# Kernel optimization log

Measured on AMD Instinct MI355X. Metric: run time of the kernel, lower is better.

The kernel has to match this reference:

```python
import jax, jax.numpy as jnp
import numpy as np

B, S, H = 2, 2048, 2048
FFN = 1024
E = 8
TOP_K = 2


def setup_inputs() -> dict:
    key = jax.random.key(0)
    ks = jax.random.split(key, 5)
    scale = 0.02
    hidden_states = jax.random.normal(ks[0], (B, S, H), dtype=jnp.float32)
    Wg = jax.random.normal(ks[1], (E, H), dtype=jnp.float32) * scale   # gate: Linear(H, E) weight
    W1 = jax.random.normal(ks[2], (E, FFN, H), dtype=jnp.float32) * scale  # stacked w1 per expert
    W3 = jax.random.normal(ks[3], (E, FFN, H), dtype=jnp.float32) * scale  # stacked w3 per expert
    W2 = jax.random.normal(ks[4], (E, H, FFN), dtype=jnp.float32) * scale  # stacked w2 per expert
    bias = jnp.zeros((E,), dtype=jnp.float32)  # e_score_correction_bias buffer
    return {"hidden_states": hidden_states, "Wg": Wg, "W1": W1, "W2": W2, "W3": W3, "bias": bias}


def reference(hidden_states, Wg, W1, W2, W3, bias):
    bsz, seq_len, hidden_dim = hidden_states.shape
    x = hidden_states.reshape(-1, hidden_dim)                 # [T, H]
    router_logits = x @ Wg.T                                  # [T, E]
    routing_weights = jax.nn.sigmoid(router_logits.astype(jnp.float32))
    scores = routing_weights + bias                           # bias only affects selection
    _, top_k_index = jax.lax.top_k(scores, TOP_K)             # [T, K]
    top_k_weights = jnp.take_along_axis(routing_weights, top_k_index, axis=1)
    top_k_weights = top_k_weights / top_k_weights.sum(axis=-1, keepdims=True)
    top_k_weights = top_k_weights.astype(x.dtype)
    # per-token per-expert combine weight (0 for non-selected experts)
    one_hot = jax.nn.one_hot(top_k_index, Wg.shape[0], dtype=x.dtype)  # [T, K, E]
    expert_w = jnp.einsum('tk,tke->te', top_k_weights, one_hot)        # [T, E]
    # SwiGLU expert MLPs applied via stacked (grouped) GEMMs
    h1 = jnp.einsum('th,efh->tef', x, W1)                     # [T, E, FFN]
    h3 = jnp.einsum('th,efh->tef', x, W3)
    g = jax.nn.silu(h1) * h3 * expert_w[:, :, None]           # scale before down-proj
    out = jnp.einsum('tef,ehf->th', g, W2)                    # weighted combine
    return out.reshape(bsz, seq_len, hidden_dim)
```

## Files before the change

kernel.cpp:

```cpp
#include <hip/hip_runtime.h>
#include <hip/hip_bf16.h>


#define T_TOK 4096
#define H_DIM 2048
#define FFN_D 1024
#define NE    8

typedef __attribute__((ext_vector_type(8))) short          bf16x8;
typedef __attribute__((ext_vector_type(4))) float          f32x4;
typedef __attribute__((ext_vector_type(4))) unsigned short us4;

__device__ __forceinline__ unsigned short f2bf(float f) {
  unsigned u = __builtin_bit_cast(unsigned, f);
  u += 0x7fffu + ((u >> 16) & 1u);
  return (unsigned short)(u >> 16);
}
__device__ __forceinline__ float bf2f(unsigned short u) {
  return __builtin_bit_cast(float, ((unsigned)u) << 16);
}
__device__ __forceinline__ void async16(const void* g, void* l) {
  __builtin_amdgcn_global_load_lds((const __attribute__((address_space(1))) void*)g,
                                   (__attribute__((address_space(3))) void*)l, 16, 0, 0);
}

__global__ void router2_kernel(const float* __restrict__ x,
                               const float* __restrict__ Wg,
                               const float* __restrict__ bias,
                               unsigned* __restrict__ epair,
                               float* __restrict__ wpair,
                               unsigned short* __restrict__ Xb) {
  const int wv   = threadIdx.x >> 6;
  const int lane = threadIdx.x & 63;
  const int t    = blockIdx.x * 4 + wv;

  const float4* xr = (const float4*)(x + (size_t)t * H_DIM);
  us4*          xb = (us4*)(Xb + (size_t)t * H_DIM);

  float acc[NE];
#pragma unroll
  for (int e = 0; e < NE; e++) acc[e] = 0.f;

#pragma unroll
  for (int j = 0; j < 8; j++) {
    int i4 = j * 64 + lane;
    float4 v = xr[i4];
    us4 d; d.x = f2bf(v.x); d.y = f2bf(v.y); d.z = f2bf(v.z); d.w = f2bf(v.w);
    xb[i4] = d;
#pragma unroll
    for (int e = 0; e < NE; e++) {
      float4 w = ((const float4*)(Wg + e * H_DIM))[i4];
      acc[e] += v.x * w.x + v.y * w.y + v.z * w.z + v.w * w.w;
    }
  }
#pragma unroll
  for (int e = 0; e < NE; e++) {
#pragma unroll
    for (int m = 32; m >= 1; m >>= 1) acc[e] += __shfl_xor(acc[e], m, 64);
  }

  if (lane == 0) {
    float sig[NE], sc[NE];
#pragma unroll
    for (int e = 0; e < NE; e++) {
      sig[e] = 1.f / (1.f + expf(-acc[e]));
      sc[e]  = sig[e] + bias[e];
    }
    int i1 = 0; float v1 = sc[0];
#pragma unroll
    for (int e = 1; e < NE; e++) if (sc[e] > v1) { v1 = sc[e]; i1 = e; }
    int i2 = -1; float v2 = -1e30f;
#pragma unroll
    for (int e = 0; e < NE; e++) if (e != i1 && sc[e] > v2) { v2 = sc[e]; i2 = e; }
    float w1 = sig[i1], w2 = sig[i2];
    float s = w1 + w2;
    epair[t] = (unsigned)i1 | ((unsigned)i2 << 8);
    wpair[2 * t]     = w1 / s;
    wpair[2 * t + 1] = w2 / s;
  }
}

#define N4_PER_W ((size_t)NE * FFN_D * H_DIM / 4)
#define NB_CONV  ((unsigned)(3 * N4_PER_W / 512))

__global__ void convert_all_kernel(const float* __restrict__ W1, unsigned short* __restrict__ W1b,
                                   const float* __restrict__ W3, unsigned short* __restrict__ W3b,
                                   const float* __restrict__ W2, unsigned short* __restrict__ W2b,
                                   const unsigned* __restrict__ epair,
                                   const float* __restrict__ wpair,
                                   int* __restrict__ cnt, int* __restrict__ base,
                                   int* __restrict__ rows, float* __restrict__ wts,
                                   int* __restrict__ t2s) {
  if (blockIdx.x < NB_CONV) {
    size_t i = (size_t)blockIdx.x * 512 + threadIdx.x;
    const float* s; unsigned short* d;
    if (i < N4_PER_W)            { s = W1; d = W1b; }
    else if (i < 2 * N4_PER_W)   { s = W3; d = W3b; i -= N4_PER_W; }
    else                         { s = W2; d = W2b; i -= 2 * N4_PER_W; }
    float4 v = ((const float4*)s)[i];
    us4 o; o.x = f2bf(v.x); o.y = f2bf(v.y); o.z = f2bf(v.z); o.w = f2bf(v.w);
    ((us4*)d)[i] = o;
    return;
  }
  const int e    = threadIdx.x >> 6;
  const int lane = threadIdx.x & 63;
  const unsigned long long ltmask = ((unsigned long long)1 << lane) - 1;
  __shared__ int cnts[NE];

  int count = 0;
  for (int c = 0; c < T_TOK; c += 64) {
    int t = c + lane;
    unsigned ep = epair[t];
    bool m1 = ((ep & 255u) == (unsigned)e);
    bool m2 = (((ep >> 8) & 255u) == (unsigned)e);
    unsigned long long b1 = __ballot(m1);
    if (m1) {
      int p = count + __popcll(b1 & ltmask);
      rows[e * T_TOK + p] = t;
      wts [e * T_TOK + p] = wpair[2 * t];
      t2s[2 * t] = (e << 12) | p;
    }
    count += __popcll(b1);
    unsigned long long b2 = __ballot(m2);
    if (m2) {
      int p = count + __popcll(b2 & ltmask);
      rows[e * T_TOK + p] = t;
      wts [e * T_TOK + p] = wpair[2 * t + 1];
      t2s[2 * t + 1] = (e << 12) | p;
    }
    count += __popcll(b2);
  }
  if (lane == 0) { cnts[e] = count; cnt[e] = count; }
  __syncthreads();
  if (threadIdx.x == 0) {
    int s = 0;
    for (int i = 0; i < NE; i++) { base[i] = s; s += cnts[i]; }
    base[NE] = s;
  }
}

__launch_bounds__(256)
__global__ void upproj_fast(const unsigned short* __restrict__ Xb,
                            const unsigned short* __restrict__ W1b,
                            const unsigned short* __restrict__ W3b,
                            const int* __restrict__ cnt,
                            const int* __restrict__ base,
                            const int* __restrict__ rows,
                            const float* __restrict__ wts,
                            unsigned short* __restrict__ G) {
  const int e  = blockIdx.z;
  const int m0 = blockIdx.y * 128;
  const int n0 = blockIdx.x * 64;
  const int ce = cnt[e];
  if (m0 >= ce) return;

  __shared__ __align__(16) unsigned short As [128 * 32];
  __shared__ __align__(16) unsigned short B1s[64 * 32];
  __shared__ __align__(16) unsigned short B3s[64 * 32];
  __shared__ int   t_ids[128];
  __shared__ float w_lds[128];

  const int tid = threadIdx.x;
  if (tid < 128) {
    int i = m0 + tid;
    if (i < ce) { t_ids[tid] = rows[e * T_TOK + i]; w_lds[tid] = wts[e * T_TOK + i]; }
    else        { t_ids[tid] = 0;                   w_lds[tid] = 0.f; }
  }
  __syncthreads();

  const int lane = tid & 63;
  const int wv   = tid >> 6;

  const unsigned short* gA[2];
#pragma unroll
  for (int c = 0; c < 2; c++) {
    int r = wv * 32 + c * 16 + (lane >> 2);
    gA[c] = Xb + (size_t)t_ids[r] * H_DIM + (lane & 3) * 8;
  }
  const size_t wrow = (size_t)(n0 + wv * 16 + (lane >> 2));
  const unsigned short* gB1 = W1b + (size_t)e * FFN_D * H_DIM + wrow * H_DIM + (lane & 3) * 8;
  const unsigned short* gB3 = W3b + (size_t)e * FFN_D * H_DIM + wrow * H_DIM + (lane & 3) * 8;
  unsigned short* lA0 = &As [(wv * 32 + 0)  * 32];
  unsigned short* lA1 = &As [(wv * 32 + 16) * 32];
  unsigned short* lB1 = &B1s[(wv * 16) * 32];
  unsigned short* lB3 = &B3s[(wv * 16) * 32];

  const int wm = (wv & 1) * 64;
  const int wn = (wv >> 1) * 32;
  const int qk = (lane >> 4) * 8;
  const int lr = lane & 15;

  f32x4 acc1[4][2], acc3[4][2];
#pragma unroll
  for (int mi = 0; mi < 4; mi++)
#pragma unroll
    for (int ni = 0; ni < 2; ni++) { acc1[mi][ni] = (f32x4)0.f; acc3[mi][ni] = (f32x4)0.f; }

  for (int kt = 0; kt < H_DIM; kt += 32) {
    async16(gA[0] + kt, lA0);
    async16(gA[1] + kt, lA1);
    async16(gB1 + kt,   lB1);
    async16(gB3 + kt,   lB3);
    __syncthreads();

    bf16x8 a[4], b1[2], b3[2];
#pragma unroll
    for (int mi = 0; mi < 4; mi++)
      a[mi] = *(const bf16x8*)&As[(wm + mi * 16 + lr) * 32 + qk];
#pragma unroll
    for (int ni = 0; ni < 2; ni++) {
      b1[ni] = *(const bf16x8*)&B1s[(wn + ni * 16 + lr) * 32 + qk];
      b3[ni] = *(const bf16x8*)&B3s[(wn + ni * 16 + lr) * 32 + qk];
    }
#pragma unroll
    for (int mi = 0; mi < 4; mi++)
#pragma unroll
      for (int ni = 0; ni < 2; ni++) {
        acc1[mi][ni] = __builtin_amdgcn_mfma_f32_16x16x32_bf16(a[mi], b1[ni], acc1[mi][ni], 0, 0, 0);
        acc3[mi][ni] = __builtin_amdgcn_mfma_f32_16x16x32_bf16(a[mi], b3[ni], acc3[mi][ni], 0, 0, 0);
      }
    __syncthreads();
  }

  const int be = base[e];
#pragma unroll
  for (int mi = 0; mi < 4; mi++)
#pragma unroll
    for (int ni = 0; ni < 2; ni++)
#pragma unroll
      for (int r = 0; r < 4; r++) {
        int row = wm + mi * 16 + (lane >> 4) * 4 + r;
        int col = wn + ni * 16 + lr;
        int i = m0 + row;
        if (i < ce) {
          float h1 = acc1[mi][ni][r];
          float h3 = acc3[mi][ni][r];
          float g  = h1 / (1.f + expf(-h1)) * h3 * w_lds[row];
          G[(size_t)(be + i) * FFN_D + n0 + col] = f2bf(g);
        }
      }
}

__launch_bounds__(256)
__global__ void downproj_fast(const unsigned short* __restrict__ G,
                              const unsigned short* __restrict__ W2b,
                              const int* __restrict__ cnt,
                              const int* __restrict__ base,
                              unsigned short* __restrict__ Gd) {
  const int e  = blockIdx.z;
  const int m0 = blockIdx.y * 128;
  const int n0 = blockIdx.x * 128;
  const int ce = cnt[e];
  if (m0 >= ce) return;
  const int be = base[e];

  __shared__ __align__(16) unsigned short As[128 * 32];
  __shared__ __align__(16) unsigned short Bs[128 * 32];

  const int tid  = threadIdx.x;
  const int lane = tid & 63;
  const int wv   = tid >> 6;

  const unsigned short* gA[2];
  const unsigned short* gB[2];
#pragma unroll
  for (int c = 0; c < 2; c++) {
    int r = m0 + wv * 32 + c * 16 + (lane >> 2);
    if (r >= ce) r = ce - 1;
    gA[c] = G + (size_t)(be + r) * FFN_D + (lane & 3) * 8;
    int rb = wv * 32 + c * 16 + (lane >> 2);
    gB[c] = W2b + (size_t)e * H_DIM * FFN_D + (size_t)(n0 + rb) * FFN_D + (lane & 3) * 8;
  }
  unsigned short* lA[2] = { &As[(wv * 32 + 0) * 32], &As[(wv * 32 + 16) * 32] };
  unsigned short* lB[2] = { &Bs[(wv * 32 + 0) * 32], &Bs[(wv * 32 + 16) * 32] };

  const int wm = (wv & 1) * 64;
  const int wn = (wv >> 1) * 64;
  const int qk = (lane >> 4) * 8;
  const int lr = lane & 15;

  f32x4 acc[4][4];
#pragma unroll
  for (int mi = 0; mi < 4; mi++)
#pragma unroll
    for (int ni = 0; ni < 4; ni++) acc[mi][ni] = (f32x4)0.f;

  for (int kt = 0; kt < FFN_D; kt += 32) {
    async16(gA[0] + kt, lA[0]);
    async16(gA[1] + kt, lA[1]);
    async16(gB[0] + kt, lB[0]);
    async16(gB[1] + kt, lB[1]);
    __syncthreads();

    bf16x8 a[4], b[4];
#pragma unroll
    for (int mi = 0; mi < 4; mi++)
      a[mi] = *(const bf16x8*)&As[(wm + mi * 16 + lr) * 32 + qk];
#pragma unroll
    for (int ni = 0; ni < 4; ni++)
      b[ni] = *(const bf16x8*)&Bs[(wn + ni * 16 + lr) * 32 + qk];
#pragma unroll
    for (int mi = 0; mi < 4; mi++)
#pragma unroll
      for (int ni = 0; ni < 4; ni++)
        acc[mi][ni] = __builtin_amdgcn_mfma_f32_16x16x32_bf16(a[mi], b[ni], acc[mi][ni], 0, 0, 0);
    __syncthreads();
  }

#pragma unroll
  for (int mi = 0; mi < 4; mi++)
#pragma unroll
    for (int ni = 0; ni < 4; ni++)
#pragma unroll
      for (int r = 0; r < 4; r++) {
        int row = wm + mi * 16 + (lane >> 4) * 4 + r;
        int col = wn + ni * 16 + lr;
        int i = m0 + row;
        if (i < ce)
          Gd[(size_t)(be + i) * H_DIM + n0 + col] = f2bf(acc[mi][ni][r]);
      }
}

__global__ void combine_kernel(const unsigned short* __restrict__ Gd,
                               const int* __restrict__ base,
                               const int* __restrict__ tok2slot,
                               float* __restrict__ out) {
  const int t = blockIdx.x;
  const int v1 = tok2slot[2 * t], v2 = tok2slot[2 * t + 1];
  const int s1 = base[v1 >> 12] + (v1 & 4095);
  const int s2 = base[v2 >> 12] + (v2 & 4095);
  const us4* r1 = (const us4*)(Gd + (size_t)s1 * H_DIM);
  const us4* r2 = (const us4*)(Gd + (size_t)s2 * H_DIM);
  float4* o = (float4*)(out + (size_t)t * H_DIM);
#pragma unroll
  for (int j = 0; j < 2; j++) {
    int i = j * 256 + threadIdx.x;
    us4 a = r1[i], b = r2[i];
    float4 r;
    r.x = bf2f(a.x) + bf2f(b.x);
    r.y = bf2f(a.y) + bf2f(b.y);
    r.z = bf2f(a.z) + bf2f(b.z);
    r.w = bf2f(a.w) + bf2f(b.w);
    o[i] = r;
  }
}

extern "C" void kernel_launch(void* const* d_in, const int* in_sizes, int n_in,
                              void* d_out, int out_size, void* d_ws, size_t ws_size,
                              hipStream_t stream) {
  (void)in_sizes; (void)n_in; (void)out_size; (void)ws_size;
  const float* x    = (const float*)d_in[0];
  const float* Wg   = (const float*)d_in[1];
  const float* W1   = (const float*)d_in[2];
  const float* W2   = (const float*)d_in[3];
  const float* W3   = (const float*)d_in[4];
  const float* bias = (const float*)d_in[5];
  float* out = (float*)d_out;

  char* ws = (char*)d_ws;
  const size_t OFF_CNT   = 0;
  const size_t OFF_BASE  = 64;
  const size_t OFF_T2S   = 1024;
  const size_t OFF_ROWS  = 65536;
  const size_t OFF_WTS   = OFF_ROWS + 131072;
  const size_t OFF_EPAIR = OFF_WTS + 131072;
  const size_t OFF_WPAIR = OFF_EPAIR + 16384;
  const size_t OFF_XB    = 1048576;
  const size_t OFF_W1B   = OFF_XB + 16777216;
  const size_t OFF_W3B   = OFF_W1B + 33554432;
  const size_t OFF_G     = OFF_W3B + 33554432;
  const size_t OFF_W2B   = OFF_G + 16777216;

  int*   cnt   = (int*)(ws + OFF_CNT);
  int*   base  = (int*)(ws + OFF_BASE);
  int*   t2s   = (int*)(ws + OFF_T2S);
  int*   rows  = (int*)(ws + OFF_ROWS);
  float* wts   = (float*)(ws + OFF_WTS);
  unsigned* epair = (unsigned*)(ws + OFF_EPAIR);
  float* wpair = (float*)(ws + OFF_WPAIR);
  unsigned short* Xb  = (unsigned short*)(ws + OFF_XB);
  unsigned short* W1b = (unsigned short*)(ws + OFF_W1B);
  unsigned short* W3b = (unsigned short*)(ws + OFF_W3B);
  unsigned short* W2b = (unsigned short*)(ws + OFF_W2B);
  unsigned short* Gd  = (unsigned short*)(ws + OFF_W1B);
  unsigned short* G   = (unsigned short*)(ws + OFF_G);

  router2_kernel<<<T_TOK / 4, 256, 0, stream>>>(x, Wg, bias, epair, wpair, Xb);

  convert_all_kernel<<<NB_CONV + 1, 512, 0, stream>>>(W1, W1b, W3, W3b, W2, W2b,
                                                      epair, wpair, cnt, base, rows, wts, t2s);

  dim3 g2(FFN_D / 64, T_TOK / 128, NE);
  upproj_fast<<<g2, 256, 0, stream>>>(Xb, W1b, W3b, cnt, base, rows, wts, G);

  dim3 g3(H_DIM / 128, T_TOK / 128, NE);
  downproj_fast<<<g3, 256, 0, stream>>>(G, W2b, cnt, base, Gd);

  combine_kernel<<<T_TOK, 256, 0, stream>>>(Gd, base, t2s, out);
}
```

Before: 461.5 us.

## Overlap weight conversion with router and up-projection kernels

Moves the W1/W3 fp32-to-bf16 conversion into the router kernel as extra blocks, and the W2 conversion into the up-projection launch as an extra z-slice, so conversion runs alongside routing and the GEMM. The compaction step becomes its own single-block kernel. This removes the serial dependency where all weight conversion had to finish before routing compaction and the up-projection could start. The trade-off is that the W2 conversion blocks now compete with GEMM blocks for CUs and memory bandwidth, and there is one extra small kernel launch.

```diff
diff --git a/kernel.cpp b/kernel.cpp
--- a/kernel.cpp
+++ b/kernel.cpp
@@ -11,6 +11,10 @@
 typedef __attribute__((ext_vector_type(4))) float          f32x4;
 typedef __attribute__((ext_vector_type(4))) unsigned short us4;
 
+#define N4_PER_W ((size_t)NE * FFN_D * H_DIM / 4)
+#define RB_ROUTER 1024u
+#define CB_CONV   8192u
+
 __device__ __forceinline__ unsigned short f2bf(float f) {
   unsigned u = __builtin_bit_cast(unsigned, f);
   u += 0x7fffu + ((u >> 16) & 1u);
@@ -24,12 +28,27 @@
                                    (__attribute__((address_space(3))) void*)l, 16, 0, 0);
 }
 
-__global__ void router2_kernel(const float* __restrict__ x,
-                               const float* __restrict__ Wg,
-                               const float* __restrict__ bias,
-                               unsigned* __restrict__ epair,
-                               float* __restrict__ wpair,
-                               unsigned short* __restrict__ Xb) {
+__global__ void router_conv_kernel(const float* __restrict__ x,
+                                   const float* __restrict__ Wg,
+                                   const float* __restrict__ bias,
+                                   unsigned* __restrict__ epair,
+                                   float* __restrict__ wpair,
+                                   unsigned short* __restrict__ Xb,
+                                   const float* __restrict__ W1, unsigned short* __restrict__ W1b,
+                                   const float* __restrict__ W3, unsigned short* __restrict__ W3b) {
+  if (blockIdx.x >= RB_ROUTER) {
+    size_t b0 = (size_t)(blockIdx.x - RB_ROUTER) * 1024;
+#pragma unroll
+    for (int k = 0; k < 4; k++) {
+      size_t i = b0 + k * 256 + threadIdx.x;
+      const float* s; unsigned short* d;
+      if (i < N4_PER_W) { s = W1; d = W1b; } else { s = W3; d = W3b; i -= N4_PER_W; }
+      float4 v = ((const float4*)s)[i];
+      us4 o; o.x = f2bf(v.x); o.y = f2bf(v.y); o.z = f2bf(v.z); o.w = f2bf(v.w);
+      ((us4*)d)[i] = o;
+    }
+    return;
+  }
   const int wv   = threadIdx.x >> 6;
   const int lane = threadIdx.x & 63;
   const int t    = blockIdx.x * 4 + wv;
@@ -80,28 +99,13 @@
   }
 }
 
-#define N4_PER_W ((size_t)NE * FFN_D * H_DIM / 4)
-#define NB_CONV  ((unsigned)(3 * N4_PER_W / 512))
-
-__global__ void convert_all_kernel(const float* __restrict__ W1, unsigned short* __restrict__ W1b,
-                                   const float* __restrict__ W3, unsigned short* __restrict__ W3b,
-                                   const float* __restrict__ W2, unsigned short* __restrict__ W2b,
-                                   const unsigned* __restrict__ epair,
-                                   const float* __restrict__ wpair,
-                                   int* __restrict__ cnt, int* __restrict__ base,
-                                   int* __restrict__ rows, float* __restrict__ wts,
-                                   int* __restrict__ t2s) {
-  if (blockIdx.x < NB_CONV) {
-    size_t i = (size_t)blockIdx.x * 512 + threadIdx.x;
-    const float* s; unsigned short* d;
-    if (i < N4_PER_W)            { s = W1; d = W1b; }
-    else if (i < 2 * N4_PER_W)   { s = W3; d = W3b; i -= N4_PER_W; }
-    else                         { s = W2; d = W2b; i -= 2 * N4_PER_W; }
-    float4 v = ((const float4*)s)[i];
-    us4 o; o.x = f2bf(v.x); o.y = f2bf(v.y); o.z = f2bf(v.z); o.w = f2bf(v.w);
-    ((us4*)d)[i] = o;
-    return;
-  }
+__global__ void compact_kernel(const unsigned* __restrict__ epair,
+                               const float* __restrict__ wpair,
+                               int* __restrict__ cnt,
+                               int* __restrict__ base,
+                               int* __restrict__ rows,
+                               float* __restrict__ wts,
+                               int* __restrict__ t2s) {
   const int e    = threadIdx.x >> 6;
   const int lane = threadIdx.x & 63;
   const unsigned long long ltmask = ((unsigned long long)1 << lane) - 1;
@@ -147,7 +151,20 @@
                             const int* __restrict__ base,
                             const int* __restrict__ rows,
                             const float* __restrict__ wts,
-                            unsigned short* __restrict__ G) {
+                            unsigned short* __restrict__ G,
+                            const float* __restrict__ W2, unsigned short* __restrict__ W2b) {
+  if (blockIdx.z == NE) {
+    size_t flat = (size_t)blockIdx.y * 16 + blockIdx.x;
+    size_t b0 = flat * 8192;
+#pragma unroll
+    for (int k = 0; k < 32; k++) {
+      size_t i = b0 + (size_t)k * 256 + threadIdx.x;
+      float4 v = ((const float4*)W2)[i];
+      us4 o; o.x = f2bf(v.x); o.y = f2bf(v.y); o.z = f2bf(v.z); o.w = f2bf(v.w);
+      ((us4*)W2b)[i] = o;
+    }
+    return;
+  }
   const int e  = blockIdx.z;
   const int m0 = blockIdx.y * 128;
   const int n0 = blockIdx.x * 64;
@@ -385,13 +402,13 @@
   unsigned short* Gd  = (unsigned short*)(ws + OFF_W1B);
   unsigned short* G   = (unsigned short*)(ws + OFF_G);
 
-  router2_kernel<<<T_TOK / 4, 256, 0, stream>>>(x, Wg, bias, epair, wpair, Xb);
-
-  convert_all_kernel<<<NB_CONV + 1, 512, 0, stream>>>(W1, W1b, W3, W3b, W2, W2b,
-                                                      epair, wpair, cnt, base, rows, wts, t2s);
-
-  dim3 g2(FFN_D / 64, T_TOK / 128, NE);
-  upproj_fast<<<g2, 256, 0, stream>>>(Xb, W1b, W3b, cnt, base, rows, wts, G);
+  router_conv_kernel<<<RB_ROUTER + CB_CONV, 256, 0, stream>>>(
+      x, Wg, bias, epair, wpair, Xb, W1, W1b, W3, W3b);
+
+  compact_kernel<<<1, 512, 0, stream>>>(epair, wpair, cnt, base, rows, wts, t2s);
+
+  dim3 g2(FFN_D / 64, T_TOK / 128, NE + 1);
+  upproj_fast<<<g2, 256, 0, stream>>>(Xb, W1b, W3b, cnt, base, rows, wts, G, W2, W2b);
 
   dim3 g3(H_DIM / 128, T_TOK / 128, NE);
   downproj_fast<<<g3, 256, 0, stream>>>(G, W2b, cnt, base, Gd);
```

After: 442.9 us. -4.0%, faster.
